# Kernel optimization log

Hardware: AMD Instinct MI355X
Metric: run time of the kernel (lower is better)

Reference implementation:

```python
import jax, jax.numpy as jnp
import numpy as np

B = 65536
HID = 128
OUT = 10


def setup_inputs() -> dict:
    key = jax.random.key(0)
    ks = jax.random.split(key, 6)
    x = jax.random.normal(ks[0], (B, 784), dtype=jnp.float32)
    conv_w = jax.random.normal(ks[1], (3, 3), dtype=jnp.float32)
    # torch Linear(676,128): weight [128,676], bias [128]
    w1 = jax.random.normal(ks[2], (HID, 26 * 26), dtype=jnp.float32) * (1.0 / np.sqrt(26 * 26))
    b1 = jax.random.normal(ks[3], (HID,), dtype=jnp.float32) * 0.01
    w2 = jax.random.normal(ks[4], (OUT, HID), dtype=jnp.float32) * (1.0 / np.sqrt(HID))
    b2 = jax.random.normal(ks[5], (OUT,), dtype=jnp.float32) * 0.01
    return {"x": x, "conv_w": conv_w, "w1": w1, "b1": b1, "w2": w2, "b2": b2}


def reference(x, conv_w, w1, b1, w2, b2):
    b = x.shape[0]
    img = x.reshape(b, 1, 28, 28)                      # NCHW, single channel
    kern = conv_w.reshape(1, 1, 3, 3)                  # OIHW
    # valid 3x3 cross-correlation (matches the elementwise-multiply-and-sum loop)
    conv = jax.lax.conv_general_dilated(
        img, kern, window_strides=(1, 1), padding="VALID",
        dimension_numbers=("NCHW", "OIHW", "NCHW"))   # [B,1,26,26]
    feat = conv.reshape(b, 26 * 26)
    h = jax.nn.relu(feat @ w1.T + b1)                  # [B,128]
    return h @ w2.T + b2                               # [B,10]
```

## Files before the change

kernel.cpp:

```cpp
#include <hip/hip_runtime.h>
#include <hip/hip_bf16.h>

#define BATCH  65536
#define KREAL  784
#define BK     64
#define NCHUNK 13
#define KPAD   (NCHUNK*BK)
#define HID    128
#define NOUT   10
#define BM     128
#define NTHR   512

using f32x4  = __attribute__((ext_vector_type(4))) float;
using short8 = __attribute__((ext_vector_type(8))) short;
using f4     = __attribute__((ext_vector_type(4))) float;

__device__ inline short f2b(float f) {
    union { __hip_bfloat16 h; short s; } u;
    u.h = __float2bfloat16(f);
    return u.s;
}

#define GLDS16(gp, lp) \
    __builtin_amdgcn_global_load_lds((const __attribute__((address_space(1))) void*)(gp), \
                                     (__attribute__((address_space(3))) void*)(lp), 16, 0, 0)

__global__ void prep_kernel(const float* __restrict__ conv_w,
                            const float* __restrict__ w1,
                            const float* __restrict__ w2,
                            unsigned short* __restrict__ weff_sw,
                            unsigned short* __restrict__ w2p)
{
    const int NW = NCHUNK * HID * BK;
    int idx = blockIdx.x * 256 + threadIdx.x;
    if (idx < NW) {
        int ic  = idx >> 13;
        int rem = idx & 8191;
        int r   = rem >> 6;
        int cc  = rem & 63;
        int g   = (cc >> 3) ^ (r & 7);
        int k   = ic * BK + g * 8 + (cc & 7);
        float acc = 0.f;
        if (k < KREAL) {
            int rr = k / 28, c = k - rr * 28;
            #pragma unroll
            for (int di = 0; di < 3; ++di) {
                int i = rr - di;
                if (i >= 0 && i < 26) {
                    #pragma unroll
                    for (int dj = 0; dj < 3; ++dj) {
                        int j = c - dj;
                        if (j >= 0 && j < 26)
                            acc = fmaf(w1[r * 676 + i * 26 + j], conv_w[di * 3 + dj], acc);
                    }
                }
            }
        }
        weff_sw[idx] = (unsigned short)f2b(acc);
    } else {
        int k = idx - NW;
        if (k < 16 * HID) {
            int o = k >> 7, c = k & 127;
            w2p[k] = (unsigned short)f2b((o < NOUT) ? w2[o * HID + c] : 0.f);
        }
    }
}

__global__ __launch_bounds__(NTHR, 4)
void fused_mlp_kernel(const float* __restrict__ x,
                      const float* __restrict__ b1,
                      const float* __restrict__ b2,
                      const unsigned short* __restrict__ weff_sw,
                      const unsigned short* __restrict__ w2p,
                      float* __restrict__ out)
{
    __shared__ __align__(16) unsigned short smem[16384];
    unsigned short* bufB0 = smem;
    unsigned short* bufB1 = smem + 8192;
    unsigned short* ldsH  = smem;

    const int tid  = threadIdx.x;
    const int wv   = tid >> 6;
    const int lane = tid & 63;
    const int lo   = lane & 15;
    const int hi   = lane >> 4;
    const int row0 = blockIdx.x * BM;
    const int wr0  = wv * 16;

    f32x4 acc[8];
    #pragma unroll
    for (int t = 0; t < 8; ++t) acc[t] = (f32x4){0.f, 0.f, 0.f, 0.f};

    const f4 fz = {0.f, 0.f, 0.f, 0.f};
    const float* arow = x + (long)(row0 + wr0 + lo) * KREAL;

    auto loadA = [&](int kbase, f4* v) {
        #pragma unroll
        for (int m = 0; m < 4; ++m) {
            int col = kbase + (m >> 1) * 32 + hi * 8 + (m & 1) * 4;
            v[m] = (col < KREAL) ? *(const f4*)(arow + col) : fz;
        }
    };
    auto stageB = [&](int ic, unsigned short* dst) {
        const char* src = (const char*)(weff_sw + ic * (HID * BK));
        int o0 = wv * 1024 + lane * 16;
        GLDS16(src + o0,        (char*)dst + wv * 1024);
        GLDS16(src + o0 + 8192, (char*)dst + wv * 1024 + 8192);
    };

    f4 av[2][4];
    loadA(0, av[0]);
    stageB(0, bufB0);

    #pragma unroll
    for (int ic = 0; ic < NCHUNK; ++ic) {
        __syncthreads();
        const unsigned short* Bc = (ic & 1) ? bufB1 : bufB0;
        unsigned short*       Bn = (ic & 1) ? bufB0 : bufB1;
        if (ic + 1 < NCHUNK) {
            stageB(ic + 1, Bn);
            loadA((ic + 1) * BK, av[(ic + 1) & 1]);
        }
        short8 af[2];
        #pragma unroll
        for (int kk = 0; kk < 2; ++kk)
            #pragma unroll
            for (int e = 0; e < 4; ++e) {
                af[kk][e]     = f2b(av[ic & 1][kk * 2][e]);
                af[kk][4 + e] = f2b(av[ic & 1][kk * 2 + 1][e]);
            }
        #pragma unroll
        for (int kk = 0; kk < 2; ++kk) {
            const int gA = kk * 4 + hi;
            #pragma unroll
            for (int t = 0; t < 8; ++t) {
                const int ob = t * 16 + lo;
                short8 bfrag = *(const short8*)&Bc[ob * BK + ((gA ^ (ob & 7)) << 3)];
                acc[t] = __builtin_amdgcn_mfma_f32_16x16x32_bf16(af[kk], bfrag, acc[t], 0, 0, 0);
            }
        }
    }

    __syncthreads();

    #pragma unroll
    for (int t = 0; t < 8; ++t) {
        float bias = b1[t * 16 + lo];
        #pragma unroll
        for (int j = 0; j < 4; ++j) {
            float hv = acc[t][j] + bias;
            hv = hv > 0.f ? hv : 0.f;
            int rloc = wr0 + hi * 4 + j;
            int col  = t * 16 + lo;
            int g    = col >> 3, e = col & 7;
            ldsH[rloc * HID + ((g ^ (rloc & 7)) << 3) + e] = (unsigned short)f2b(hv);
        }
    }

    f32x4 acc2 = (f32x4){0.f, 0.f, 0.f, 0.f};
    #pragma unroll
    for (int kk = 0; kk < 4; ++kk) {
        int r = wr0 + lo;
        int g = kk * 4 + hi;
        short8 ha = *(const short8*)&ldsH[r * HID + ((g ^ (r & 7)) << 3)];
        short8 wb = *(const short8*)(w2p + lo * HID + kk * 32 + hi * 8);
        acc2 = __builtin_amdgcn_mfma_f32_16x16x32_bf16(ha, wb, acc2, 0, 0, 0);
    }
    if (lo < NOUT) {
        float bb = b2[lo];
        #pragma unroll
        for (int j = 0; j < 4; ++j) {
            int grow = row0 + wr0 + hi * 4 + j;
            out[grow * NOUT + lo] = acc2[j] + bb;
        }
    }
}

extern "C" void kernel_launch(void* const* d_in, const int* in_sizes, int n_in,
                              void* d_out, int out_size, void* d_ws, size_t ws_size,
                              hipStream_t stream)
{
    const float* x      = (const float*)d_in[0];
    const float* conv_w = (const float*)d_in[1];
    const float* w1     = (const float*)d_in[2];
    const float* b1     = (const float*)d_in[3];
    const float* w2     = (const float*)d_in[4];
    const float* b2     = (const float*)d_in[5];
    float* out = (float*)d_out;

    unsigned short* weff_sw = (unsigned short*)d_ws;
    unsigned short* w2p     = weff_sw + NCHUNK * HID * BK;

    const int prep_total = NCHUNK * HID * BK + 16 * HID;
    prep_kernel<<<(prep_total + 255) / 256, 256, 0, stream>>>(conv_w, w1, w2, weff_sw, w2p);
    fused_mlp_kernel<<<BATCH / BM, NTHR, 0, stream>>>(x, b1, b2, weff_sw, w2p, out);
}
```

Before: 46.83 us.

## Load MFMA-fragment-ordered weights directly from global, dropping LDS staging

The prep kernel now writes the folded conv+linear weights pre-arranged in MFMA fragment order, so each lane reads its B fragment with one contiguous 16-byte global load. The main kernel no longer double-buffers weight chunks in LDS and removes the per-chunk barriers. The block shrinks to 64 rows and 4 waves, which gives more blocks and lowers LDS use. The cost is that every wave re-reads the full weight matrix from L2/cache instead of sharing it through LDS, and the software prefetch of the next A chunk is gone.

```diff
diff --git a/kernel.cpp b/kernel.cpp
--- a/kernel.cpp
+++ b/kernel.cpp
@@ -5,11 +5,10 @@
 #define KREAL  784
 #define BK     64
 #define NCHUNK 13
-#define KPAD   (NCHUNK*BK)
 #define HID    128
 #define NOUT   10
-#define BM     128
-#define NTHR   512
+#define BM     64
+#define NTHR   256
 
 using f32x4  = __attribute__((ext_vector_type(4))) float;
 using short8 = __attribute__((ext_vector_type(8))) short;
@@ -21,25 +20,25 @@
     return u.s;
 }
 
-#define GLDS16(gp, lp) \
-    __builtin_amdgcn_global_load_lds((const __attribute__((address_space(1))) void*)(gp), \
-                                     (__attribute__((address_space(3))) void*)(lp), 16, 0, 0)
+#define NWF (NCHUNK*2*8*4*16*8)
+#define NW2 (4*4*16*8)
 
 __global__ void prep_kernel(const float* __restrict__ conv_w,
                             const float* __restrict__ w1,
                             const float* __restrict__ w2,
-                            unsigned short* __restrict__ weff_sw,
-                            unsigned short* __restrict__ w2p)
+                            unsigned short* __restrict__ weff_f,
+                            unsigned short* __restrict__ w2f)
 {
-    const int NW = NCHUNK * HID * BK;
     int idx = blockIdx.x * 256 + threadIdx.x;
-    if (idx < NW) {
-        int ic  = idx >> 13;
-        int rem = idx & 8191;
-        int r   = rem >> 6;
-        int cc  = rem & 63;
-        int g   = (cc >> 3) ^ (r & 7);
-        int k   = ic * BK + g * 8 + (cc & 7);
+    if (idx < NWF) {
+        int e  = idx & 7;
+        int lo = (idx >> 3) & 15;
+        int hi = (idx >> 7) & 3;
+        int t  = (idx >> 9) & 7;
+        int kk = (idx >> 12) & 1;
+        int ic = idx >> 13;
+        int row = t * 16 + lo;
+        int k   = ic * BK + kk * 32 + hi * 8 + e;
         float acc = 0.f;
         if (k < KREAL) {
             int rr = k / 28, c = k - rr * 28;
@@ -51,17 +50,21 @@
                     for (int dj = 0; dj < 3; ++dj) {
                         int j = c - dj;
                         if (j >= 0 && j < 26)
-                            acc = fmaf(w1[r * 676 + i * 26 + j], conv_w[di * 3 + dj], acc);
+                            acc = fmaf(w1[row * 676 + i * 26 + j], conv_w[di * 3 + dj], acc);
                     }
                 }
             }
         }
-        weff_sw[idx] = (unsigned short)f2b(acc);
+        weff_f[idx] = (unsigned short)f2b(acc);
     } else {
-        int k = idx - NW;
-        if (k < 16 * HID) {
-            int o = k >> 7, c = k & 127;
-            w2p[k] = (unsigned short)f2b((o < NOUT) ? w2[o * HID + c] : 0.f);
+        int k2 = idx - NWF;
+        if (k2 < NW2) {
+            int e  = k2 & 7;
+            int lo = (k2 >> 3) & 15;
+            int hi = (k2 >> 7) & 3;
+            int kk = k2 >> 9;
+            float v = (lo < NOUT) ? w2[lo * HID + kk * 32 + hi * 8 + e] : 0.f;
+            w2f[k2] = (unsigned short)f2b(v);
         }
     }
 }
@@ -70,14 +73,11 @@
 void fused_mlp_kernel(const float* __restrict__ x,
                       const float* __restrict__ b1,
                       const float* __restrict__ b2,
-                      const unsigned short* __restrict__ weff_sw,
-                      const unsigned short* __restrict__ w2p,
+                      const unsigned short* __restrict__ weff_f,
+                      const unsigned short* __restrict__ w2f,
                       float* __restrict__ out)
 {
-    __shared__ __align__(16) unsigned short smem[16384];
-    unsigned short* bufB0 = smem;
-    unsigned short* bufB1 = smem + 8192;
-    unsigned short* ldsH  = smem;
+    __shared__ __align__(16) unsigned short ldsH[BM * HID];
 
     const int tid  = threadIdx.x;
     const int wv   = tid >> 6;
@@ -93,55 +93,35 @@
 
     const f4 fz = {0.f, 0.f, 0.f, 0.f};
     const float* arow = x + (long)(row0 + wr0 + lo) * KREAL;
+    const unsigned short* bfr = weff_f + ((long)hi * 16 + lo) * 8;
 
-    auto loadA = [&](int kbase, f4* v) {
+    #pragma unroll
+    for (int ic = 0; ic < NCHUNK; ++ic) {
+        const int kbase = ic * BK;
+        f4 av[4];
         #pragma unroll
         for (int m = 0; m < 4; ++m) {
             int col = kbase + (m >> 1) * 32 + hi * 8 + (m & 1) * 4;
-            v[m] = (col < KREAL) ? *(const f4*)(arow + col) : fz;
-        }
-    };
-    auto stageB = [&](int ic, unsigned short* dst) {
-        const char* src = (const char*)(weff_sw + ic * (HID * BK));
-        int o0 = wv * 1024 + lane * 16;
-        GLDS16(src + o0,        (char*)dst + wv * 1024);
-        GLDS16(src + o0 + 8192, (char*)dst + wv * 1024 + 8192);
-    };
-
-    f4 av[2][4];
-    loadA(0, av[0]);
-    stageB(0, bufB0);
-
-    #pragma unroll
-    for (int ic = 0; ic < NCHUNK; ++ic) {
-        __syncthreads();
-        const unsigned short* Bc = (ic & 1) ? bufB1 : bufB0;
-        unsigned short*       Bn = (ic & 1) ? bufB0 : bufB1;
-        if (ic + 1 < NCHUNK) {
-            stageB(ic + 1, Bn);
-            loadA((ic + 1) * BK, av[(ic + 1) & 1]);
+            av[m] = (col < KREAL) ? *(const f4*)(arow + col) : fz;
         }
         short8 af[2];
         #pragma unroll
         for (int kk = 0; kk < 2; ++kk)
             #pragma unroll
             for (int e = 0; e < 4; ++e) {
-                af[kk][e]     = f2b(av[ic & 1][kk * 2][e]);
-                af[kk][4 + e] = f2b(av[ic & 1][kk * 2 + 1][e]);
+                af[kk][e]     = f2b(av[kk * 2][e]);
+                af[kk][4 + e] = f2b(av[kk * 2 + 1][e]);
             }
         #pragma unroll
         for (int kk = 0; kk < 2; ++kk) {
-            const int gA = kk * 4 + hi;
+            const unsigned short* bs = bfr + ((long)(ic * 2 + kk) * 8) * 512;
             #pragma unroll
             for (int t = 0; t < 8; ++t) {
-                const int ob = t * 16 + lo;
-                short8 bfrag = *(const short8*)&Bc[ob * BK + ((gA ^ (ob & 7)) << 3)];
+                short8 bfrag = *(const short8*)(bs + (long)t * 512);
                 acc[t] = __builtin_amdgcn_mfma_f32_16x16x32_bf16(af[kk], bfrag, acc[t], 0, 0, 0);
             }
         }
     }
-
-    __syncthreads();
 
     #pragma unroll
     for (int t = 0; t < 8; ++t) {
@@ -163,7 +143,7 @@
         int r = wr0 + lo;
         int g = kk * 4 + hi;
         short8 ha = *(const short8*)&ldsH[r * HID + ((g ^ (r & 7)) << 3)];
-        short8 wb = *(const short8*)(w2p + lo * HID + kk * 32 + hi * 8);
+        short8 wb = *(const short8*)(w2f + (((kk * 4 + hi) * 16 + lo) << 3));
         acc2 = __builtin_amdgcn_mfma_f32_16x16x32_bf16(ha, wb, acc2, 0, 0, 0);
     }
     if (lo < NOUT) {
@@ -188,10 +168,10 @@
     const float* b2     = (const float*)d_in[5];
     float* out = (float*)d_out;
 
-    unsigned short* weff_sw = (unsigned short*)d_ws;
-    unsigned short* w2p     = weff_sw + NCHUNK * HID * BK;
+    unsigned short* weff_f = (unsigned short*)d_ws;
+    unsigned short* w2f    = weff_f + NWF;
 
-    const int prep_total = NCHUNK * HID * BK + 16 * HID;
-    prep_kernel<<<(prep_total + 255) / 256, 256, 0, stream>>>(conv_w, w1, w2, weff_sw, w2p);
-    fused_mlp_kernel<<<BATCH / BM, NTHR, 0, stream>>>(x, b1, b2, weff_sw, w2p, out);
+    const int prep_total = NWF + NW2;
+    prep_kernel<<<(prep_total + 255) / 256, 256, 0, stream>>>(conv_w, w1, w2, weff_f, w2f);
+    fused_mlp_kernel<<<BATCH / BM, NTHR, 0, stream>>>(x, b1, b2, weff_f, w2f, out);
 }
```

Result: slower. 77.17 us (+64.8%).

## Stage A tiles via async global-to-LDS loads and halve block tile

Applied to the files above, without the earlier changes.

The activation rows of x are now staged into double-buffered LDS through global_load_lds with an XOR swizzle, instead of going through registers. The block tile shrinks to 64 rows with 256 threads, and LDS grows to 64KB with launch bounds lowered to 2 blocks per SM. The w2 fragment is repacked so each lane's load is contiguous. The aim is to overlap the x stream asynchronously and relieve register pressure. The cost is lower occupancy from the larger LDS footprint, and each block now reloads the full B weights for only half as many rows.

```diff
diff --git a/kernel.cpp b/kernel.cpp
--- a/kernel.cpp
+++ b/kernel.cpp
@@ -5,11 +5,10 @@
 #define KREAL  784
 #define BK     64
 #define NCHUNK 13
-#define KPAD   (NCHUNK*BK)
 #define HID    128
 #define NOUT   10
-#define BM     128
-#define NTHR   512
+#define BM     64
+#define NTHR   256
 
 using f32x4  = __attribute__((ext_vector_type(4))) float;
 using short8 = __attribute__((ext_vector_type(8))) short;
@@ -25,15 +24,17 @@
     __builtin_amdgcn_global_load_lds((const __attribute__((address_space(1))) void*)(gp), \
                                      (__attribute__((address_space(3))) void*)(lp), 16, 0, 0)
 
+#define NWB (NCHUNK*HID*BK)
+#define NW2 (4*4*16*8)
+
 __global__ void prep_kernel(const float* __restrict__ conv_w,
                             const float* __restrict__ w1,
                             const float* __restrict__ w2,
                             unsigned short* __restrict__ weff_sw,
-                            unsigned short* __restrict__ w2p)
+                            unsigned short* __restrict__ w2f)
 {
-    const int NW = NCHUNK * HID * BK;
     int idx = blockIdx.x * 256 + threadIdx.x;
-    if (idx < NW) {
+    if (idx < NWB) {
         int ic  = idx >> 13;
         int rem = idx & 8191;
         int r   = rem >> 6;
@@ -58,26 +59,32 @@
         }
         weff_sw[idx] = (unsigned short)f2b(acc);
     } else {
-        int k = idx - NW;
-        if (k < 16 * HID) {
-            int o = k >> 7, c = k & 127;
-            w2p[k] = (unsigned short)f2b((o < NOUT) ? w2[o * HID + c] : 0.f);
-        }
-    }
-}
-
-__global__ __launch_bounds__(NTHR, 4)
+        int k2 = idx - NWB;
+        if (k2 < NW2) {
+            int e  = k2 & 7;
+            int lo = (k2 >> 3) & 15;
+            int hi = (k2 >> 7) & 3;
+            int kk = k2 >> 9;
+            float v = (lo < NOUT) ? w2[lo * HID + kk * 32 + hi * 8 + e] : 0.f;
+            w2f[k2] = (unsigned short)f2b(v);
+        }
+    }
+}
+
+__global__ __launch_bounds__(NTHR, 2)
 void fused_mlp_kernel(const float* __restrict__ x,
                       const float* __restrict__ b1,
                       const float* __restrict__ b2,
                       const unsigned short* __restrict__ weff_sw,
-                      const unsigned short* __restrict__ w2p,
+                      const unsigned short* __restrict__ w2f,
                       float* __restrict__ out)
 {
-    __shared__ __align__(16) unsigned short smem[16384];
-    unsigned short* bufB0 = smem;
-    unsigned short* bufB1 = smem + 8192;
-    unsigned short* ldsH  = smem;
+    __shared__ __align__(16) unsigned char smem[65536];
+    float*          bufA0 = (float*)smem;
+    float*          bufA1 = (float*)(smem + 16384);
+    unsigned short* bufB0 = (unsigned short*)(smem + 32768);
+    unsigned short* bufB1 = (unsigned short*)(smem + 49152);
+    unsigned short* ldsH  = (unsigned short*)smem;
 
     const int tid  = threadIdx.x;
     const int wv   = tid >> 6;
@@ -91,52 +98,54 @@
     #pragma unroll
     for (int t = 0; t < 8; ++t) acc[t] = (f32x4){0.f, 0.f, 0.f, 0.f};
 
-    const f4 fz = {0.f, 0.f, 0.f, 0.f};
-    const float* arow = x + (long)(row0 + wr0 + lo) * KREAL;
-
-    auto loadA = [&](int kbase, f4* v) {
-        #pragma unroll
-        for (int m = 0; m < 4; ++m) {
-            int col = kbase + (m >> 1) * 32 + hi * 8 + (m & 1) * 4;
-            v[m] = (col < KREAL) ? *(const f4*)(arow + col) : fz;
+    const char* abase = (const char*)(x + (long)(row0 + wr0 + hi) * KREAL);
+    auto stageA = [&](int ic, float* dst) {
+        #pragma unroll
+        for (int j = 0; j < 4; ++j) {
+            int sg = lo ^ (j * 4 + hi);
+            int ce = ic * BK + sg * 4;
+            int cb = (ce < KREAL) ? ce : 0;
+            GLDS16(abase + (long)j * 4 * KREAL * 4 + cb * 4,
+                   (char*)dst + (wr0 + j * 4) * 256);
         }
     };
     auto stageB = [&](int ic, unsigned short* dst) {
-        const char* src = (const char*)(weff_sw + ic * (HID * BK));
-        int o0 = wv * 1024 + lane * 16;
-        GLDS16(src + o0,        (char*)dst + wv * 1024);
-        GLDS16(src + o0 + 8192, (char*)dst + wv * 1024 + 8192);
+        const char* src = (const char*)(weff_sw + (long)ic * (HID * BK));
+        #pragma unroll
+        for (int j = 0; j < 4; ++j)
+            GLDS16(src + wv * 4096 + j * 1024 + lane * 16,
+                   (char*)dst + wv * 4096 + j * 1024);
     };
 
-    f4 av[2][4];
-    loadA(0, av[0]);
+    stageA(0, bufA0);
     stageB(0, bufB0);
 
     #pragma unroll
     for (int ic = 0; ic < NCHUNK; ++ic) {
         __syncthreads();
+        const float*          Ac = (ic & 1) ? bufA1 : bufA0;
         const unsigned short* Bc = (ic & 1) ? bufB1 : bufB0;
-        unsigned short*       Bn = (ic & 1) ? bufB0 : bufB1;
         if (ic + 1 < NCHUNK) {
-            stageB(ic + 1, Bn);
-            loadA((ic + 1) * BK, av[(ic + 1) & 1]);
-        }
-        short8 af[2];
-        #pragma unroll
-        for (int kk = 0; kk < 2; ++kk)
+            stageA(ic + 1, (ic & 1) ? bufA0 : bufA1);
+            stageB(ic + 1, (ic & 1) ? bufB0 : bufB1);
+        }
+        const int r = wr0 + lo;
+        #pragma unroll
+        for (int kk = 0; kk < 2; ++kk) {
+            const int G = kk * 4 + hi;
+            f4 a0 = *(const f4*)((const char*)Ac + r * 256 + ((( 2 * G    ) ^ lo) << 4));
+            f4 a1 = *(const f4*)((const char*)Ac + r * 256 + (((2 * G + 1) ^ lo) << 4));
+            short8 af;
             #pragma unroll
             for (int e = 0; e < 4; ++e) {
-                af[kk][e]     = f2b(av[ic & 1][kk * 2][e]);
-                af[kk][4 + e] = f2b(av[ic & 1][kk * 2 + 1][e]);
+                af[e]     = f2b(a0[e]);
+                af[4 + e] = f2b(a1[e]);
             }
-        #pragma unroll
-        for (int kk = 0; kk < 2; ++kk) {
-            const int gA = kk * 4 + hi;
             #pragma unroll
             for (int t = 0; t < 8; ++t) {
                 const int ob = t * 16 + lo;
-                short8 bfrag = *(const short8*)&Bc[ob * BK + ((gA ^ (ob & 7)) << 3)];
-                acc[t] = __builtin_amdgcn_mfma_f32_16x16x32_bf16(af[kk], bfrag, acc[t], 0, 0, 0);
+                short8 bfrag = *(const short8*)&Bc[ob * BK + ((G ^ (ob & 7)) << 3)];
+                acc[t] = __builtin_amdgcn_mfma_f32_16x16x32_bf16(af, bfrag, acc[t], 0, 0, 0);
             }
         }
     }
@@ -163,7 +172,7 @@
         int r = wr0 + lo;
         int g = kk * 4 + hi;
         short8 ha = *(const short8*)&ldsH[r * HID + ((g ^ (r & 7)) << 3)];
-        short8 wb = *(const short8*)(w2p + lo * HID + kk * 32 + hi * 8);
+        short8 wb = *(const short8*)(w2f + (((kk * 4 + hi) * 16 + lo) << 3));
         acc2 = __builtin_amdgcn_mfma_f32_16x16x32_bf16(ha, wb, acc2, 0, 0, 0);
     }
     if (lo < NOUT) {
@@ -189,9 +198,9 @@
     float* out = (float*)d_out;
 
     unsigned short* weff_sw = (unsigned short*)d_ws;
-    unsigned short* w2p     = weff_sw + NCHUNK * HID * BK;
-
-    const int prep_total = NCHUNK * HID * BK + 16 * HID;
-    prep_kernel<<<(prep_total + 255) / 256, 256, 0, stream>>>(conv_w, w1, w2, weff_sw, w2p);
-    fused_mlp_kernel<<<BATCH / BM, NTHR, 0, stream>>>(x, b1, b2, weff_sw, w2p, out);
-}
+    unsigned short* w2f     = weff_sw + NWB;
+
+    const int prep_total = NWB + NW2;
+    prep_kernel<<<(prep_total + 255) / 256, 256, 0, stream>>>(conv_w, w1, w2, weff_sw, w2f);
+    fused_mlp_kernel<<<BATCH / BM, NTHR, 0, stream>>>(x, b1, b2, weff_sw, w2f, out);
+}
```

Result: faster. 44.04 us (-5.9%).
